# Performance work log

Hardware: AMD Instinct MI355X
Metric: run time of the kernel (lower is better)

The kernel has to match this reference:

```python
import jax, jax.numpy as jnp
import numpy as np

WINDOW = 512
STEP = WINDOW // 2


def hamming_window(n):
    # torch.hamming_window default is periodic=True: 0.54 - 0.46*cos(2*pi*k/n)
    return (0.54 - 0.46 * jnp.cos(2.0 * jnp.pi * jnp.arange(n) / n)).astype(jnp.float32)


def fft_convolve(a, b):
    # ortho-normalized rfft spectra, irfft, crop back to n samples.
    n = a.shape[-1]
    pa = jnp.pad(a, [(0, 0)] * (a.ndim - 1) + [(0, n)])
    pb = jnp.pad(b, [(0, 0)] * (b.ndim - 1) + [(0, n)])
    spec = jnp.fft.rfft(pa, axis=-1, norm='ortho') * jnp.fft.rfft(pb, axis=-1, norm='ortho')
    return jnp.fft.irfft(spec, n=2 * n, axis=-1, norm='ortho')[..., :n]


def fft_shift(a, shift):
    # repo's fft_shift: fractional shift via phase ramp in rfft domain of the
    n = a.shape[-1]
    shift_samples = shift * n * 0.5  # [..., 1]
    pa = jnp.pad(a, [(0, 0)] * (a.ndim - 1) + [(0, n)])
    spec = jnp.fft.rfft(pa, axis=-1, norm='ortho')  # [..., n+1]
    n_coeffs = spec.shape[-1]
    ramp = (jnp.arange(n_coeffs) * 2j * jnp.pi) / n_coeffs
    phase = jnp.exp(-ramp * shift_samples)  # broadcast over last dim
    return jnp.fft.irfft(spec * phase, n=2 * n, axis=-1, norm='ortho')


def setup_inputs() -> dict:
    key = jax.random.key(0)
    k1, k2 = jax.random.split(key)
    B, n = 4, 32768
    recon = jax.random.normal(k1, (B, 1, n), dtype=jnp.float32)
    target = jax.random.normal(k2, (B, 1, n), dtype=jnp.float32)
    return {"recon": recon, "target": target}


def reference(recon, target):
    batch = recon.shape[0]
    n_samples = recon.shape[-1]
    n_frames = (n_samples - WINDOW) // STEP + 1  # unfold(-1, 512, 256)

    # unfold: gather overlapping frames [B, n_frames, WINDOW]
    idx = jnp.arange(n_frames)[:, None] * STEP + jnp.arange(WINDOW)[None, :]
    frames = recon[:, 0, :][:, idx]  # [B, n_frames, WINDOW]
    windowed = (frames * hamming_window(WINDOW))[:, None, :, :]  # [B,1,F,W]

    # zero-pad each frame up to n_samples (the torch.cat with zeros)
    windowed = jnp.pad(windowed, ((0, 0), (0, 0), (0, 0), (0, n_samples - WINDOW)))

    # FFT cross-correlation surrogate against the full target
    fm = fft_convolve(windowed, target[:, :, None, :])[..., :n_samples]  # [B,1,F,n]

    positions = jnp.argmax(fm, axis=-1, keepdims=True).astype(jnp.float32) / n_samples

    positioned = fft_shift(windowed, positions)[..., :n_samples]  # [B,1,F,n]
    positioned = jnp.sum(positioned, axis=2).reshape(batch, 1, n_samples)

    return jnp.mean((positioned - target) ** 2)
```

## Files before the change

### kernel.cpp

```cpp
#include <hip/hip_runtime.h>
#include <math.h>

#define N_SAMP   32768
#define WINDOW   512
#define STEP     256
#define NFRAMES  127
#define NB       4
#define RTRUNC   1280
#define NSLAB    32
#define BPAD     776
#define HW       3104
#define VSTRIDE  193

#define WS_WF   0
#define WS_WFH  260096
#define WS_WFL  391168
#define WS_PV   522240
#define WS_M    587776
#define WS_CNT  588288
#define WS_LIST 588304
#define WS_H    592400
#define WS_PART 2169232

typedef _Float16 f16x8 __attribute__((ext_vector_type(8)));
typedef float f32x16 __attribute__((ext_vector_type(16)));

#define SW(L) ((L) ^ (((L) >> 3) & 7))

#define FMA4(A, LO, HI)                                           \
    A.x = fmaf(c.x, HI.x, A.x); A.x = fmaf(c.y, LO.w, A.x);       \
    A.x = fmaf(c.z, LO.z, A.x); A.x = fmaf(c.w, LO.y, A.x);       \
    A.y = fmaf(c.x, HI.y, A.y); A.y = fmaf(c.y, HI.x, A.y);       \
    A.y = fmaf(c.z, LO.w, A.y); A.y = fmaf(c.w, LO.z, A.y);       \
    A.z = fmaf(c.x, HI.z, A.z); A.z = fmaf(c.y, HI.y, A.z);       \
    A.z = fmaf(c.z, HI.x, A.z); A.z = fmaf(c.w, LO.w, A.z);       \
    A.w = fmaf(c.x, HI.w, A.w); A.w = fmaf(c.y, HI.z, A.w);       \
    A.w = fmaf(c.z, HI.y, A.w); A.w = fmaf(c.w, HI.x, A.w);

__global__ __launch_bounds__(256) void k_wf(const float* __restrict__ recon,
                                            float* __restrict__ wf,
                                            _Float16* __restrict__ wfh) {
    int e = blockIdx.x * 256 + threadIdx.x;
    int w     = e & 511;
    int bf128 = e >> 9;
    int f = bf128 & 127;
    int b = bf128 >> 7;
    float val = 0.f;
    if (f < NFRAMES) {
        float ham = 0.54f - 0.46f * (float)cos((double)w * (M_PI / 256.0));
        val = ham * recon[b * N_SAMP + f * STEP + w];
        wf[(b * NFRAMES + f) * 512 + w] = val;
    }
    size_t tr = (((size_t)b * 64 + (w >> 3)) * 128 + f) * 8 + (w & 7);
    wfh[tr] = (_Float16)val;
}

__global__ __launch_bounds__(256, 4) void k_argmax_mfma(
        const float* __restrict__ tgt,
        const _Float16* __restrict__ wfh,
        float* __restrict__ pv) {
    __shared__ _Float16 sbh[8 * BPAD];
    const int tid   = threadIdx.x;
    const int chunk = blockIdx.x & 127;
    const int half  = (blockIdx.x >> 7) & 1;
    const int b     = blockIdx.x >> 8;
    const int T0    = chunk * 256;
    const int TB    = T0 + 255;
    const float* tb = tgt + b * N_SAMP;

    for (int oc = tid; oc < 768; oc += 256) {
        int r = oc / 96, s = oc - r * 96;
        int base = TB - r - 8 * s;
        _Float16 h8[8];
#pragma unroll
        for (int j = 0; j < 8; ++j) {
            int t = base - j;
            h8[j] = (_Float16)((t >= 0) ? tb[t] : 0.0f);
        }
        *(f16x8*)&sbh[r * BPAD + 8 * s] = *(f16x8*)h8;
    }
    __syncthreads();

    const int wv  = tid >> 6;
    const int q   = (tid >> 5) & 1;
    const int cl  = tid & 31;
    const int nt0 = 2 * wv;
    const int rp  = 7 - (cl & 7);
    const _Float16* Ah0 = wfh + ((size_t)b * 64) * 1024 + (half * 64 + cl) * 8;

    f32x16 acc00 = (f32x16)(0.f);
    f32x16 acc01 = (f32x16)(0.f);
    f32x16 acc10 = (f32x16)(0.f);
    f32x16 acc11 = (f32x16)(0.f);

    int off = q * 1024;
    int ea  = rp * BPAD + (255 - 32 * nt0 - cl + 8 * q - rp);
    f16x8 a0  = *(const f16x8*)(Ah0 + off);
    f16x8 a1  = *(const f16x8*)(Ah0 + off + 256);
    f16x8 bh0 = *(const f16x8*)&sbh[ea];
    f16x8 bh1 = *(const f16x8*)&sbh[ea - 32];
#pragma unroll
    for (int k0 = 0; k0 < 512; k0 += 16) {
        f16x8 a0n  = *(const f16x8*)(Ah0 + off + 2048);
        f16x8 a1n  = *(const f16x8*)(Ah0 + off + 2304);
        f16x8 bh0n = *(const f16x8*)&sbh[ea + 16];
        f16x8 bh1n = *(const f16x8*)&sbh[ea - 16];
        acc00 = __builtin_amdgcn_mfma_f32_32x32x16_f16(a0, bh0, acc00, 0, 0, 0);
        acc01 = __builtin_amdgcn_mfma_f32_32x32x16_f16(a0, bh1, acc01, 0, 0, 0);
        acc10 = __builtin_amdgcn_mfma_f32_32x32x16_f16(a1, bh0, acc10, 0, 0, 0);
        acc11 = __builtin_amdgcn_mfma_f32_32x32x16_f16(a1, bh1, acc11, 0, 0, 0);
        a0 = a0n; a1 = a1n; bh0 = bh0n; bh1 = bh1n;
        off += 2048; ea += 16;
    }

    __syncthreads();
    float* sval = (float*)sbh;
#pragma unroll
    for (int r = 0; r < 16; ++r) {
        float v0 = fmaxf(acc00[r], acc01[r]);
        float v1 = fmaxf(acc10[r], acc11[r]);
#pragma unroll
        for (int mm = 1; mm <= 16; mm <<= 1) {
            v0 = fmaxf(v0, __shfl_xor(v0, mm));
            v1 = fmaxf(v1, __shfl_xor(v1, mm));
        }
        if (cl == 0) {
            int row = (r & 3) + 8 * (r >> 2) + 4 * q;
            sval[row * 4 + wv]        = v0;
            sval[(32 + row) * 4 + wv] = v1;
        }
    }
    __syncthreads();
    if (tid < 64) {
        float v = fmaxf(fmaxf(sval[tid * 4], sval[tid * 4 + 1]),
                        fmaxf(sval[tid * 4 + 2], sval[tid * 4 + 3]));
        pv[((size_t)b * 128 + half * 64 + tid) * 128 + chunk] = v;
    }
}

__global__ __launch_bounds__(256) void k_vmax(const float* __restrict__ tgt,
                                              const float* __restrict__ wf,
                                              const float* __restrict__ pv,
                                              int* __restrict__ marr) {
    __shared__ __align__(16) float stg[4 * VSTRIDE * 4];
    __shared__ float rv[256];
    __shared__ int   ri[256];
    __shared__ int   clist[32];
    __shared__ int   ccnt;
    const int tid  = threadIdx.x;
    const int lane = tid & 63;
    const int wv   = tid >> 6;
    const int fr   = blockIdx.x;
    const int b    = fr / NFRAMES;
    const int f    = fr - b * NFRAMES;
    const float* prow = pv + ((size_t)b * 128 + f) * 128;
    const float* tb   = tgt + b * N_SAMP;
    const float4* wcg = (const float4*)(wf + (size_t)fr * 512);

    float mv = (tid < 128) ? prow[tid] : -3.4e38f;
    rv[tid] = mv;
    __syncthreads();
    for (int s = 128; s > 0; s >>= 1) {
        if (tid < s) rv[tid] = fmaxf(rv[tid], rv[tid + s]);
        __syncthreads();
    }
    float m0 = rv[0];
    if (tid == 0) ccnt = 0;
    __syncthreads();
    float eps = 0.012f * fabsf(m0) + 1e-3f;
    if (tid < 128 && mv >= m0 - eps) {
        int k = atomicAdd(&ccnt, 1);
        if (k < 32) clist[k] = tid;
    }
    __syncthreads();
    int nc = ccnt;
    int total = (nc <= 32) ? nc : 128;
    float bestv = -3.4e38f; int bestt = 0x7fffffff;
    float* myg = stg + wv * (VSTRIDE * 4);

    for (int ci = wv; ci < total; ci += 4) {
        int c2 = (nc <= 32) ? clist[ci] : ci;
        int T0 = c2 * 256;
        for (int e = lane; e < 192; e += 64) {
            int A = T0 - 512 + 4 * e;
            float4 vq = (A >= 0 && A < N_SAMP) ? *(const float4*)(tb + A)
                                               : make_float4(0.f, 0.f, 0.f, 0.f);
            *(float4*)(myg + 4 * e) = vq;
        }
        float4 acc = make_float4(0.f, 0.f, 0.f, 0.f);
        float4 lo = *(const float4*)(myg + 4 * (lane + 127));
        float4 hi = *(const float4*)(myg + 4 * (lane + 128));
        for (int g = 0; g < 127; ++g) {
            float4 nl = *(const float4*)(myg + 4 * (lane + 126 - g));
            const float4 c = wcg[g];
            FMA4(acc, lo, hi);
            hi = lo; lo = nl;
        }
        {
            const float4 c = wcg[127];
            FMA4(acc, lo, hi);
        }
        int tt = T0 + 4 * lane;
        if (acc.x > bestv || (acc.x == bestv && tt     < bestt)) { bestv = acc.x; bestt = tt;     }
        if (acc.y > bestv || (acc.y == bestv && tt + 1 < bestt)) { bestv = acc.y; bestt = tt + 1; }
        if (acc.z > bestv || (acc.z == bestv && tt + 2 < bestt)) { bestv = acc.z; bestt = tt + 2; }
        if (acc.w > bestv || (acc.w == bestv && tt + 3 < bestt)) { bestv = acc.w; bestt = tt + 3; }
    }
    rv[tid] = bestv; ri[tid] = bestt;
    __syncthreads();
    for (int s = 128; s > 0; s >>= 1) {
        if (tid < s) {
            float v2 = rv[tid + s]; int i2 = ri[tid + s];
            if (v2 > rv[tid] || (v2 == rv[tid] && i2 < ri[tid])) {
                rv[tid] = v2; ri[tid] = i2;
            }
        }
        __syncthreads();
    }
    if (tid == 0) marr[fr] = ri[0];
}

__global__ __launch_bounds__(256) void k_coef(const int* __restrict__ marr,
                                              float* __restrict__ hbuf) {
    const int bf  = blockIdx.x;
    const int tid = threadIdx.x;
    const double invD = 1.0 / 2147549184.0;
    const float  sd   = 4.7936899603827e-05f;
    const float  trf  = (float)(RTRUNC + 4) / 65536.0f;
    int m = marr[bf];
    int p = (int)rint((double)m * (32768.0 / 32769.0));
    int jlo = p - (RTRUNC + 8); if (jlo < -512) jlo = -512; jlo &= ~3;
    float* hr = hbuf + (size_t)bf * HW;
    if (m == 0) {
        for (int k4 = tid; k4 < 776; k4 += 256) {
            int j0 = jlo + 4 * k4;
            float4 vq = make_float4((j0 == 0) ? 1.0f : 0.0f, 0.f, 0.f, 0.f);
            *(float4*)(hr + 4 * k4) = vq;
        }
        return;
    }
    double md32768 = (double)m * 32768.0;
    double sp = sin((double)m * (M_PI / 32769.0));
    float Cp = (float)(sp * (1.0 / 65536.0));
    if (m & 1) Cp = -Cp;
    float Cn = -Cp;
    for (int k4 = tid; k4 < 776; k4 += 256) {
        int j0 = jlo + 4 * k4;
        double A0 = (double)j0 * 32769.0 - md32768;
        double rA0 = A0 * invD;
        float f0v = (float)(rA0 - rint(rA0));
        float4 vq;
        if (fabsf(f0v) > trf) {
            vq = make_float4(0.f, 0.f, 0.f, 0.f);
        } else if (fabsf(f0v) < 6.2e-5f) {
#pragma unroll
            for (int k = 0; k < 4; ++k) {
                double rA = (A0 + (double)k * 32769.0) * invD;
                float ff = (float)(rA - rint(rA));
                float r2;
                if (ff == 0.0f) r2 = 65535.0f;
                else {
                    float s, c2;
                    __sincosf((float)M_PI * ff, &s, &c2);
                    r2 = c2 * __builtin_amdgcn_rcpf(s);
                }
                ((float*)&vq)[k] = ((k & 1) ? Cn : Cp) * r2;
            }
        } else {
            float s, c2;
            __sincosf((float)M_PI * f0v, &s, &c2);
            vq.x = Cp * (c2 * __builtin_amdgcn_rcpf(s));
            float s1 = fmaf(c2, sd, s);
            float c1 = fmaf(-s, sd, c2);
            vq.y = Cn * (c1 * __builtin_amdgcn_rcpf(s1));
            float s2 = fmaf(c1, sd, s1);
            float cc2 = fmaf(-s1, sd, c1);
            vq.z = Cp * (cc2 * __builtin_amdgcn_rcpf(s2));
            float s3 = fmaf(cc2, sd, s2);
            float c3 = fmaf(-s2, sd, cc2);
            vq.w = Cn * (c3 * __builtin_amdgcn_rcpf(s3));
        }
        *(float4*)(hr + 4 * k4) = vq;
    }
}

__global__ __launch_bounds__(256) void k_sched(const int* __restrict__ marr,
                                               int* __restrict__ list,
                                               int* __restrict__ cnt,
                                               int nslab) {
    __shared__ int scnt[64];
    __shared__ int total;
    const int tid = threadIdx.x;
    if (tid < 64) scnt[tid] = 0;
    if (tid == 0) total = 0;
    __syncthreads();
    const int RT8 = RTRUNC + 8;
    for (int bf = tid; bf < NB * NFRAMES; bf += 256) {
        int b = bf / NFRAMES;
        int m = marr[bf];
        int p = (int)rint((double)m * (32768.0 / 32769.0));
        int lo = p - RT8;        if (lo < 0) lo = 0;
        int hi = p + RT8 + 511;  if (hi > N_SAMP - 1) hi = N_SAMP - 1;
        int r0 = lo >> 11, r1 = hi >> 11;
        for (int r = r0; r <= r1; ++r) {
            int bc = (b << 4) | r;
            int s = atomicAdd(&scnt[bc], 1);
            int k = atomicAdd(&total, 1);
            list[k] = (bf << 16) | (r << 8) | s;
        }
    }
    __syncthreads();
    int n = total;
    for (int k = tid; k < n; k += 256) {
        int v = list[k];
        int bf = (v >> 16) & 0x3fff;
        int r = (v >> 8) & 15;
        int b = bf / NFRAMES;
        if (scnt[(b << 4) | r] > nslab) list[k] = v | (1 << 30);
    }
    if (tid == 0) {
        int mx = 0;
        for (int i = 0; i < 64; ++i) mx = (scnt[i] > mx) ? scnt[i] : mx;
        cnt[0] = n;
        cnt[1] = (mx > nslab) ? nslab : mx;
    }
}

#define LDBLK2(nn) (*(const float4*)(s_h + 4 * SW(Lt + (nn))))
#define CB3(g, A, Bq, Cq)                                         \
    {                                                             \
        float4 tnew = LDBLK2(126 - (g));                          \
        const float4 c = wc[(g)];                                 \
        FMA4(acc0, w[A], w[Bq]); FMA4(acc1, w[Bq], w[Cq]);        \
        w[Cq] = tnew;                                             \
    }
#define CB3_NL(g, A, Bq, Cq)                                      \
    {                                                             \
        const float4 c = wc[(g)];                                 \
        FMA4(acc0, w[A], w[Bq]); FMA4(acc1, w[Bq], w[Cq]);        \
    }

__global__ __launch_bounds__(256, 8) void k_shift_acc(const float* __restrict__ wf,
                                                      const int* __restrict__ marr,
                                                      const int* __restrict__ list,
                                                      const int* __restrict__ cnt,
                                                      const float* __restrict__ hbuf,
                                                      float* __restrict__ part,
                                                      int slabmask) {
    __shared__ __align__(16) float s_h[2560];
    const int tid = threadIdx.x;
    const int Lt  = 2 * tid;
    const int Ltw = (tid >> 6) * 128;
    const int n   = cnt[0];

    for (int se = blockIdx.x; se < n; se += gridDim.x) {
        int v     = list[se];
        int bf    = (v >> 16) & 0x3fff;
        int r     = (v >> 8) & 15;
        int slot  = v & 255;
        int isat  = (v >> 30) & 1;
        int b     = bf / NFRAMES;
        int t0s   = r << 11;
        const float4* __restrict__ wc = (const float4*)(wf + bf * 512);

        int m  = marr[bf];
        int pr = (int)rint((double)m * (32768.0 / 32769.0));
        int jlo = pr - (RTRUNC + 8); if (jlo < -512) jlo = -512; jlo &= ~3;
        int kb0 = ((t0s - 512) - jlo) >> 2;
        const float4* __restrict__ hb = (const float4*)(hbuf + (size_t)bf * HW);

        __syncthreads();
        for (int e4 = tid; e4 < 640; e4 += 256) {
            int kb = kb0 + e4;
            float4 vq = (kb >= 0 && kb < 776) ? hb[kb]
                                              : make_float4(0.f, 0.f, 0.f, 0.f);
            *(float4*)(s_h + 4 * SW(e4)) = vq;
        }
        __syncthreads();

        int blo = (pr - (RTRUNC + 8) - (t0s - 512)) >> 2;
        int bhi = (pr + (RTRUNC + 8) - (t0s - 512)) >> 2;
        if (blo < 0) blo = 0;
        if (bhi > 639) bhi = 639;

        float4 acc0 = make_float4(0.f, 0.f, 0.f, 0.f);
        float4 acc1 = acc0;

        int gmin = Ltw + 127 - bhi; if (gmin < 0) gmin = 0;
        int gmax = Ltw + 255 - blo; if (gmax > 127) gmax = 127;
        if (gmin <= gmax) {
            int go0 = gmin / 3;
            bool tail = (gmax >= 126);
            int goE = tail ? 42 : (gmax / 3 + 1);
            int gb0 = 3 * go0;
            float4 w[3];
            w[0] = LDBLK2(127 - gb0);
            w[1] = LDBLK2(128 - gb0);
            w[2] = LDBLK2(129 - gb0);
            for (int go = go0; go < goE && go < 42; ++go) {
                const int gb = 3 * go;
                CB3(gb + 0, 0, 1, 2);
                CB3(gb + 1, 2, 0, 1);
                CB3(gb + 2, 1, 2, 0);
            }
            if (tail) { CB3(126, 0, 1, 2); CB3_NL(127, 2, 0, 1); }
        }

        int slab = slot & slabmask;
        float* ob = part + (size_t)slab * (NB * N_SAMP) + b * N_SAMP + t0s;
        if (!isat) {
            *(float4*)(ob + 8 * tid)     = acc0;
            *(float4*)(ob + 8 * tid + 4) = acc1;
        } else {
            float* p0 = ob + 8 * tid;
            atomicAdd(p0 + 0, acc0.x); atomicAdd(p0 + 1, acc0.y);
            atomicAdd(p0 + 2, acc0.z); atomicAdd(p0 + 3, acc0.w);
            atomicAdd(p0 + 4, acc1.x); atomicAdd(p0 + 5, acc1.y);
            atomicAdd(p0 + 6, acc1.z); atomicAdd(p0 + 7, acc1.w);
        }
    }
}

__global__ __launch_bounds__(256) void k_mse(const float* __restrict__ part,
                                             const float* __restrict__ tgt,
                                             float* __restrict__ out,
                                             const int* __restrict__ cnt,
                                             int nslab) {
    __shared__ float sred[4];
    int e = blockIdx.x * 256 + threadIdx.x;
    int ng = cnt[1];
    if (ng > nslab) ng = nslab;
    float s0 = 0.f, s1 = 0.f, s2 = 0.f, s3 = 0.f;
    int g = 0;
    for (; g + 4 <= ng; g += 4) {
        s0 += part[(size_t)(g + 0) * (NB * N_SAMP) + e];
        s1 += part[(size_t)(g + 1) * (NB * N_SAMP) + e];
        s2 += part[(size_t)(g + 2) * (NB * N_SAMP) + e];
        s3 += part[(size_t)(g + 3) * (NB * N_SAMP) + e];
    }
    for (; g < ng; ++g)
        s0 += part[(size_t)g * (NB * N_SAMP) + e];
    float s = (s0 + s1) + (s2 + s3);
    float d = s - tgt[e];
    float v = d * d;
#pragma unroll
    for (int off = 32; off > 0; off >>= 1) v += __shfl_down(v, off, 64);
    int lane = threadIdx.x & 63, wid = threadIdx.x >> 6;
    if (lane == 0) sred[wid] = v;
    __syncthreads();
    if (threadIdx.x == 0) {
        float sm = sred[0] + sred[1] + sred[2] + sred[3];
        atomicAdd(out, sm * (1.0f / 131072.0f));
    }
}

extern "C" void kernel_launch(void* const* d_in, const int* in_sizes, int n_in,
                              void* d_out, int out_size, void* d_ws, size_t ws_size,
                              hipStream_t stream) {
    const float* recon = (const float*)d_in[0];
    const float* tgt   = (const float*)d_in[1];
    float* out = (float*)d_out;
    float* W   = (float*)d_ws;

    float*     wf   = W + WS_WF;
    _Float16*  wfh  = (_Float16*)(W + WS_WFH);
    float*     pv   = W + WS_PV;
    int*       marr = (int*)(W + WS_M);
    int*       cnt  = (int*)(W + WS_CNT);
    int*       list = (int*)(W + WS_LIST);
    float*     hbuf = W + WS_H;
    float*     part = W + WS_PART;

    int nslab = NSLAB;
    while (nslab > 1 &&
           ((size_t)WS_PART + (size_t)nslab * NB * N_SAMP) * sizeof(float) > ws_size)
        nslab >>= 1;

    hipMemsetAsync(out, 0, sizeof(float), stream);
    hipMemsetAsync(part, 0, (size_t)nslab * NB * N_SAMP * sizeof(float), stream);

    k_wf<<<1024, 256, 0, stream>>>(recon, wf, wfh);
    k_argmax_mfma<<<1024, 256, 0, stream>>>(tgt, wfh, pv);
    k_vmax<<<NB * NFRAMES, 256, 0, stream>>>(tgt, wf, pv, marr);
    k_coef<<<NB * NFRAMES, 256, 0, stream>>>(marr, hbuf);
    k_sched<<<1, 256, 0, stream>>>(marr, list, cnt, nslab);
    k_shift_acc<<<2048, 256, 0, stream>>>(wf, marr, list, cnt, hbuf, part, nslab - 1);
    k_mse<<<512, 256, 0, stream>>>(part, tgt, out, cnt, nslab);
}
```

Before: 174.7 us.

## Fold scheduling into coef kernel and unroll shift accumulation by five

```diff
diff --git a/kernel.cpp b/kernel.cpp
--- a/kernel.cpp
+++ b/kernel.cpp
@@ -221,9 +221,54 @@
 }
 
 __global__ __launch_bounds__(256) void k_coef(const int* __restrict__ marr,
-                                              float* __restrict__ hbuf) {
+                                              float* __restrict__ hbuf,
+                                              int* __restrict__ list,
+                                              int* __restrict__ cnt,
+                                              int nslab,
+                                              float* __restrict__ out) {
+    const int tid = threadIdx.x;
+
+    if (blockIdx.x == NB * NFRAMES) {
+        __shared__ int scnt[64];
+        __shared__ int total;
+        if (tid == 0) out[0] = 0.0f;
+        if (tid < 64) scnt[tid] = 0;
+        if (tid == 0) total = 0;
+        __syncthreads();
+        const int RT8 = RTRUNC + 8;
+        for (int bf = tid; bf < NB * NFRAMES; bf += 256) {
+            int b = bf / NFRAMES;
+            int m = marr[bf];
+            int p = (int)rint((double)m * (32768.0 / 32769.0));
+            int lo = p - RT8;        if (lo < 0) lo = 0;
+            int hi = p + RT8 + 511;  if (hi > N_SAMP - 1) hi = N_SAMP - 1;
+            int r0 = lo >> 11, r1 = hi >> 11;
+            for (int r = r0; r <= r1; ++r) {
+                int bc = (b << 4) | r;
+                int s = atomicAdd(&scnt[bc], 1);
+                int k = atomicAdd(&total, 1);
+                list[k] = (bf << 16) | (r << 8) | s;
+            }
+        }
+        __syncthreads();
+        int n = total;
+        for (int k = tid; k < n; k += 256) {
+            int v = list[k];
+            int bf = (v >> 16) & 0x3fff;
+            int r = (v >> 8) & 15;
+            int b = bf / NFRAMES;
+            if (scnt[(b << 4) | r] > nslab) list[k] = v | (1 << 30);
+        }
+        if (tid == 0) {
+            int mx = 0;
+            for (int i = 0; i < 64; ++i) mx = (scnt[i] > mx) ? scnt[i] : mx;
+            cnt[0] = n;
+            cnt[1] = (mx > nslab) ? nslab : mx;
+        }
+        return;
+    }
+
     const int bf  = blockIdx.x;
-    const int tid = threadIdx.x;
     const double invD = 1.0 / 2147549184.0;
     const float  sd   = 4.7936899603827e-05f;
     const float  trf  = (float)(RTRUNC + 4) / 65536.0f;
@@ -284,60 +329,14 @@
     }
 }
 
-__global__ __launch_bounds__(256) void k_sched(const int* __restrict__ marr,
-                                               int* __restrict__ list,
-                                               int* __restrict__ cnt,
-                                               int nslab) {
-    __shared__ int scnt[64];
-    __shared__ int total;
-    const int tid = threadIdx.x;
-    if (tid < 64) scnt[tid] = 0;
-    if (tid == 0) total = 0;
-    __syncthreads();
-    const int RT8 = RTRUNC + 8;
-    for (int bf = tid; bf < NB * NFRAMES; bf += 256) {
-        int b = bf / NFRAMES;
-        int m = marr[bf];
-        int p = (int)rint((double)m * (32768.0 / 32769.0));
-        int lo = p - RT8;        if (lo < 0) lo = 0;
-        int hi = p + RT8 + 511;  if (hi > N_SAMP - 1) hi = N_SAMP - 1;
-        int r0 = lo >> 11, r1 = hi >> 11;
-        for (int r = r0; r <= r1; ++r) {
-            int bc = (b << 4) | r;
-            int s = atomicAdd(&scnt[bc], 1);
-            int k = atomicAdd(&total, 1);
-            list[k] = (bf << 16) | (r << 8) | s;
-        }
-    }
-    __syncthreads();
-    int n = total;
-    for (int k = tid; k < n; k += 256) {
-        int v = list[k];
-        int bf = (v >> 16) & 0x3fff;
-        int r = (v >> 8) & 15;
-        int b = bf / NFRAMES;
-        if (scnt[(b << 4) | r] > nslab) list[k] = v | (1 << 30);
-    }
-    if (tid == 0) {
-        int mx = 0;
-        for (int i = 0; i < 64; ++i) mx = (scnt[i] > mx) ? scnt[i] : mx;
-        cnt[0] = n;
-        cnt[1] = (mx > nslab) ? nslab : mx;
-    }
-}
-
-#define LDBLK2(nn) (*(const float4*)(s_h + 4 * SW(Lt + (nn))))
-#define CB3(g, A, Bq, Cq)                                         \
-    {                                                             \
-        float4 tnew = LDBLK2(126 - (g));                          \
-        const float4 c = wc[(g)];                                 \
-        FMA4(acc0, w[A], w[Bq]); FMA4(acc1, w[Bq], w[Cq]);        \
-        w[Cq] = tnew;                                             \
-    }
-#define CB3_NL(g, A, Bq, Cq)                                      \
-    {                                                             \
-        const float4 c = wc[(g)];                                 \
-        FMA4(acc0, w[A], w[Bq]); FMA4(acc1, w[Bq], w[Cq]);        \
+#define LDB5(nn) (*(const float4*)(s_h + 4 * SW((nn) + 8)))
+#define CB5(K, LOs, MIDs, HIs)                                    \
+    if (gb + (K) <= gmax) {                                       \
+        float4 tnew = LDB5(Lt + 124 - gb - (K));                  \
+        const float4 c = c##K;                                    \
+        FMA4(acc0, LOs, MIDs); FMA4(acc1, MIDs, HIs);             \
+        HIs = tnew;                                               \
+        c##K = wc[(gb + (K) + 5 <= 127) ? (gb + (K) + 5) : 127];  \
     }
 
 __global__ __launch_bounds__(256, 8) void k_shift_acc(const float* __restrict__ wf,
@@ -347,7 +346,7 @@
                                                       const float* __restrict__ hbuf,
                                                       float* __restrict__ part,
                                                       int slabmask) {
-    __shared__ __align__(16) float s_h[2560];
+    __shared__ __align__(16) float s_h[2624];
     const int tid = threadIdx.x;
     const int Lt  = 2 * tid;
     const int Ltw = (tid >> 6) * 128;
@@ -374,7 +373,7 @@
             int kb = kb0 + e4;
             float4 vq = (kb >= 0 && kb < 776) ? hb[kb]
                                               : make_float4(0.f, 0.f, 0.f, 0.f);
-            *(float4*)(s_h + 4 * SW(e4)) = vq;
+            *(float4*)(s_h + 4 * SW(e4 + 8)) = vq;
         }
         __syncthreads();
 
@@ -389,21 +388,24 @@
         int gmin = Ltw + 127 - bhi; if (gmin < 0) gmin = 0;
         int gmax = Ltw + 255 - blo; if (gmax > 127) gmax = 127;
         if (gmin <= gmax) {
-            int go0 = gmin / 3;
-            bool tail = (gmax >= 126);
-            int goE = tail ? 42 : (gmax / 3 + 1);
-            int gb0 = 3 * go0;
-            float4 w[3];
-            w[0] = LDBLK2(127 - gb0);
-            w[1] = LDBLK2(128 - gb0);
-            w[2] = LDBLK2(129 - gb0);
-            for (int go = go0; go < goE && go < 42; ++go) {
-                const int gb = 3 * go;
-                CB3(gb + 0, 0, 1, 2);
-                CB3(gb + 1, 2, 0, 1);
-                CB3(gb + 2, 1, 2, 0);
+            int gb0 = (gmin / 5) * 5;
+            float4 w0 = LDB5(Lt + 129 - gb0);
+            float4 w1 = LDB5(Lt + 128 - gb0);
+            float4 w2 = LDB5(Lt + 127 - gb0);
+            float4 w3 = LDB5(Lt + 126 - gb0);
+            float4 w4 = LDB5(Lt + 125 - gb0);
+            float4 c0 = wc[gb0];
+            float4 c1 = wc[(gb0 + 1 <= 127) ? gb0 + 1 : 127];
+            float4 c2 = wc[(gb0 + 2 <= 127) ? gb0 + 2 : 127];
+            float4 c3 = wc[(gb0 + 3 <= 127) ? gb0 + 3 : 127];
+            float4 c4 = wc[(gb0 + 4 <= 127) ? gb0 + 4 : 127];
+            for (int gb = gb0; gb <= gmax; gb += 5) {
+                CB5(0, w2, w1, w0);
+                CB5(1, w3, w2, w1);
+                CB5(2, w4, w3, w2);
+                CB5(3, w0, w4, w3);
+                CB5(4, w1, w0, w4);
             }
-            if (tail) { CB3(126, 0, 1, 2); CB3_NL(127, 2, 0, 1); }
         }
 
         int slab = slot & slabmask;
@@ -476,14 +478,12 @@
            ((size_t)WS_PART + (size_t)nslab * NB * N_SAMP) * sizeof(float) > ws_size)
         nslab >>= 1;
 
-    hipMemsetAsync(out, 0, sizeof(float), stream);
     hipMemsetAsync(part, 0, (size_t)nslab * NB * N_SAMP * sizeof(float), stream);
 
     k_wf<<<1024, 256, 0, stream>>>(recon, wf, wfh);
     k_argmax_mfma<<<1024, 256, 0, stream>>>(tgt, wfh, pv);
     k_vmax<<<NB * NFRAMES, 256, 0, stream>>>(tgt, wf, pv, marr);
-    k_coef<<<NB * NFRAMES, 256, 0, stream>>>(marr, hbuf);
-    k_sched<<<1, 256, 0, stream>>>(marr, list, cnt, nslab);
+    k_coef<<<NB * NFRAMES + 1, 256, 0, stream>>>(marr, hbuf, list, cnt, nslab, out);
     k_shift_acc<<<2048, 256, 0, stream>>>(wf, marr, list, cnt, hbuf, part, nslab - 1);
     k_mse<<<512, 256, 0, stream>>>(part, tgt, out, cnt, nslab);
 }
```

Result: no change. 177.8 us (+1.8%).

## Fold memsets and scheduler kernel into neighbouring kernels, stage target via LDS

Applied to the files above, without the earlier changes.

```diff
diff --git a/kernel.cpp b/kernel.cpp
--- a/kernel.cpp
+++ b/kernel.cpp
@@ -39,7 +39,9 @@
 
 __global__ __launch_bounds__(256) void k_wf(const float* __restrict__ recon,
                                             float* __restrict__ wf,
-                                            _Float16* __restrict__ wfh) {
+                                            _Float16* __restrict__ wfh,
+                                            float* __restrict__ part,
+                                            int nslab) {
     int e = blockIdx.x * 256 + threadIdx.x;
     int w     = e & 511;
     int bf128 = e >> 9;
@@ -53,6 +55,10 @@
     }
     size_t tr = (((size_t)b * 64 + (w >> 3)) * 128 + f) * 8 + (w & 7);
     wfh[tr] = (_Float16)val;
+    float4* p4 = (float4*)part;
+    int nq = nslab * 32768;
+    for (int q = e; q < nq; q += 262144)
+        p4[q] = make_float4(0.f, 0.f, 0.f, 0.f);
 }
 
 __global__ __launch_bounds__(256, 4) void k_argmax_mfma(
@@ -60,6 +66,7 @@
         const _Float16* __restrict__ wfh,
         float* __restrict__ pv) {
     __shared__ _Float16 sbh[8 * BPAD];
+    __shared__ __align__(16) float stf[768];
     const int tid   = threadIdx.x;
     const int chunk = blockIdx.x & 127;
     const int half  = (blockIdx.x >> 7) & 1;
@@ -68,15 +75,20 @@
     const int TB    = T0 + 255;
     const float* tb = tgt + b * N_SAMP;
 
+    if (tid < 192) {
+        int A = TB - 767 + 4 * tid;
+        float4 vq = (A >= 0) ? *(const float4*)(tb + A)
+                             : make_float4(0.f, 0.f, 0.f, 0.f);
+        *(float4*)(stf + 4 * tid) = vq;
+    }
+    __syncthreads();
     for (int oc = tid; oc < 768; oc += 256) {
         int r = oc / 96, s = oc - r * 96;
-        int base = TB - r - 8 * s;
+        int y0 = 767 - r - 8 * s;
         _Float16 h8[8];
 #pragma unroll
-        for (int j = 0; j < 8; ++j) {
-            int t = base - j;
-            h8[j] = (_Float16)((t >= 0) ? tb[t] : 0.0f);
-        }
+        for (int j = 0; j < 8; ++j)
+            h8[j] = (_Float16)stf[y0 - j];
         *(f16x8*)&sbh[r * BPAD + 8 * s] = *(f16x8*)h8;
     }
     __syncthreads();
@@ -221,9 +233,54 @@
 }
 
 __global__ __launch_bounds__(256) void k_coef(const int* __restrict__ marr,
-                                              float* __restrict__ hbuf) {
+                                              float* __restrict__ hbuf,
+                                              int* __restrict__ list,
+                                              int* __restrict__ cnt,
+                                              int nslab,
+                                              float* __restrict__ out) {
+    const int tid = threadIdx.x;
+
+    if (blockIdx.x == NB * NFRAMES) {
+        __shared__ int scnt[64];
+        __shared__ int total;
+        if (tid == 0) out[0] = 0.0f;
+        if (tid < 64) scnt[tid] = 0;
+        if (tid == 0) total = 0;
+        __syncthreads();
+        const int RT8 = RTRUNC + 8;
+        for (int bf = tid; bf < NB * NFRAMES; bf += 256) {
+            int b = bf / NFRAMES;
+            int m = marr[bf];
+            int p = (int)rint((double)m * (32768.0 / 32769.0));
+            int lo = p - RT8;        if (lo < 0) lo = 0;
+            int hi = p + RT8 + 511;  if (hi > N_SAMP - 1) hi = N_SAMP - 1;
+            int r0 = lo >> 11, r1 = hi >> 11;
+            for (int r = r0; r <= r1; ++r) {
+                int bc = (b << 4) | r;
+                int s = atomicAdd(&scnt[bc], 1);
+                int k = atomicAdd(&total, 1);
+                list[k] = (bf << 16) | (r << 8) | s;
+            }
+        }
+        __syncthreads();
+        int n = total;
+        for (int k = tid; k < n; k += 256) {
+            int v = list[k];
+            int bf = (v >> 16) & 0x3fff;
+            int r = (v >> 8) & 15;
+            int b = bf / NFRAMES;
+            if (scnt[(b << 4) | r] > nslab) list[k] = v | (1 << 30);
+        }
+        if (tid == 0) {
+            int mx = 0;
+            for (int i = 0; i < 64; ++i) mx = (scnt[i] > mx) ? scnt[i] : mx;
+            cnt[0] = n;
+            cnt[1] = (mx > nslab) ? nslab : mx;
+        }
+        return;
+    }
+
     const int bf  = blockIdx.x;
-    const int tid = threadIdx.x;
     const double invD = 1.0 / 2147549184.0;
     const float  sd   = 4.7936899603827e-05f;
     const float  trf  = (float)(RTRUNC + 4) / 65536.0f;
@@ -284,48 +341,6 @@
     }
 }
 
-__global__ __launch_bounds__(256) void k_sched(const int* __restrict__ marr,
-                                               int* __restrict__ list,
-                                               int* __restrict__ cnt,
-                                               int nslab) {
-    __shared__ int scnt[64];
-    __shared__ int total;
-    const int tid = threadIdx.x;
-    if (tid < 64) scnt[tid] = 0;
-    if (tid == 0) total = 0;
-    __syncthreads();
-    const int RT8 = RTRUNC + 8;
-    for (int bf = tid; bf < NB * NFRAMES; bf += 256) {
-        int b = bf / NFRAMES;
-        int m = marr[bf];
-        int p = (int)rint((double)m * (32768.0 / 32769.0));
-        int lo = p - RT8;        if (lo < 0) lo = 0;
-        int hi = p + RT8 + 511;  if (hi > N_SAMP - 1) hi = N_SAMP - 1;
-        int r0 = lo >> 11, r1 = hi >> 11;
-        for (int r = r0; r <= r1; ++r) {
-            int bc = (b << 4) | r;
-            int s = atomicAdd(&scnt[bc], 1);
-            int k = atomicAdd(&total, 1);
-            list[k] = (bf << 16) | (r << 8) | s;
-        }
-    }
-    __syncthreads();
-    int n = total;
-    for (int k = tid; k < n; k += 256) {
-        int v = list[k];
-        int bf = (v >> 16) & 0x3fff;
-        int r = (v >> 8) & 15;
-        int b = bf / NFRAMES;
-        if (scnt[(b << 4) | r] > nslab) list[k] = v | (1 << 30);
-    }
-    if (tid == 0) {
-        int mx = 0;
-        for (int i = 0; i < 64; ++i) mx = (scnt[i] > mx) ? scnt[i] : mx;
-        cnt[0] = n;
-        cnt[1] = (mx > nslab) ? nslab : mx;
-    }
-}
-
 #define LDBLK2(nn) (*(const float4*)(s_h + 4 * SW(Lt + (nn))))
 #define CB3(g, A, Bq, Cq)                                         \
     {                                                             \
@@ -476,14 +491,10 @@
            ((size_t)WS_PART + (size_t)nslab * NB * N_SAMP) * sizeof(float) > ws_size)
         nslab >>= 1;
 
-    hipMemsetAsync(out, 0, sizeof(float), stream);
-    hipMemsetAsync(part, 0, (size_t)nslab * NB * N_SAMP * sizeof(float), stream);
-
-    k_wf<<<1024, 256, 0, stream>>>(recon, wf, wfh);
+    k_wf<<<1024, 256, 0, stream>>>(recon, wf, wfh, part, nslab);
     k_argmax_mfma<<<1024, 256, 0, stream>>>(tgt, wfh, pv);
     k_vmax<<<NB * NFRAMES, 256, 0, stream>>>(tgt, wf, pv, marr);
-    k_coef<<<NB * NFRAMES, 256, 0, stream>>>(marr, hbuf);
-    k_sched<<<1, 256, 0, stream>>>(marr, list, cnt, nslab);
+    k_coef<<<NB * NFRAMES + 1, 256, 0, stream>>>(marr, hbuf, list, cnt, nslab, out);
     k_shift_acc<<<2048, 256, 0, stream>>>(wf, marr, list, cnt, hbuf, part, nslab - 1);
     k_mse<<<512, 256, 0, stream>>>(part, tgt, out, cnt, nslab);
 }
```

Result: faster. 157.2 us (-10.0%).
